# Optimization experiments

Hardware: AMD Instinct MI355X
Metric: run time of the kernel (lower is better)

## Reference

```python
import jax, jax.numpy as jnp
from jax import lax
import numpy as np

VTH = 0.2
DECAY = 0.25            # LIF membrane decay used by pcdmd slayers.LIFSpike (STBP-style)
DT = 0.001              # norse default integration step
TAU_SYN_INV = 200.0     # norse LSNNParameters defaults
TAU_MEM_INV = 100.0
TAU_ADAPT_INV = 1.0 / 700.0
BETA = 0.0              # module sets beta=0 (no threshold adaptation jumps)
ALPHA = 100.0           # SuperSpike surrogate slope (norse 'super' method)

@jax.custom_vjp
def spike_rect(v):
    # Heaviside forward, rectangular surrogate backward (STBP)
    return (v > 0).astype(v.dtype)

def _sr_fwd(v):
    return spike_rect(v), v

def _sr_bwd(v, g):
    return (g * (jnp.abs(v) < 0.5).astype(g.dtype),)

spike_rect.defvjp(_sr_fwd, _sr_bwd)

@jax.custom_vjp
def spike_super(v):
    # Heaviside forward, SuperSpike surrogate backward (norse 'super')
    return (v > 0).astype(v.dtype)

def _ss_fwd(v):
    return spike_super(v), v

def _ss_bwd(v, g):
    return (g / (ALPHA * jnp.abs(v) + 1.0) ** 2,)

spike_super.defvjp(_ss_fwd, _ss_bwd)

def lif_spike(x):
    # x: [..., T] -> spike train [..., T]
    # u_t = DECAY * u_{t-1} * (1 - o_{t-1}) + x_t ; o_t = H(u_t - VTH)
    xT = jnp.moveaxis(x, -1, 0)  # [T, ...]
    u0 = jnp.zeros(xT.shape[1:], x.dtype)
    def step(carry, xt):
        u, o = carry
        u = DECAY * u * (1.0 - o) + xt
        o = spike_rect(u - VTH)
        return (u, o), o
    _, out = lax.scan(step, (u0, u0), xT)
    return jnp.moveaxis(out, 0, -1)

def lsnn_recurrent(x, w_in, w_rec):
    # x: [T, B, H] input spikes; norse LSNNRecurrent lsnn_step with beta=0, v_th=VTH
    x_in = jnp.einsum('tbh,oh->tbo', x, w_in)  # input current, hoisted out of scan
    B, H = x.shape[1], w_in.shape[0]
    z0 = jnp.zeros((B, H), x.dtype)
    state0 = (z0, z0, z0, jnp.full((B, H), VTH, x.dtype))  # z, v, i, b (b starts at v_th)
    def step(state, xt):
        z, v, i, b = state
        i_jump = i + xt + z @ w_rec.T
        v_dec = v + DT * TAU_MEM_INV * (-v + i_jump)          # v_leak = 0
        i_dec = i_jump - DT * TAU_SYN_INV * i_jump
        b_dec = b + DT * TAU_ADAPT_INV * (VTH - b)
        z_new = spike_super(v_dec - b_dec)
        v_new = (1.0 - z_new) * v_dec                          # v_reset = 0
        b_new = b_dec + z_new * TAU_ADAPT_INV * BETA
        return (z_new, v_new, i_dec, b_new), z_new
    _, out = lax.scan(step, state0, x_in)
    return out  # [T, B, H]

def setup_inputs() -> dict:
    key = jax.random.key(0)
    ks = jax.random.split(key, 7)
    B, T = 64, 8192
    EEG_C, AUD_C, H, OUT = 64, 1, 10, 2
    x = jax.random.normal(ks[0], (B, 1, EEG_C + 2 * AUD_C, T), jnp.float32)
    s_in = 1.0 / float(np.sqrt(EEG_C))
    s_h = 1.0 / float(np.sqrt(H))
    return {
        'x': x,
        'w_front': jax.random.uniform(ks[1], (H, EEG_C), jnp.float32, -s_in, s_in),
        'b_front': jax.random.uniform(ks[2], (H,), jnp.float32, -s_in, s_in),
        'w_in': jax.random.uniform(ks[3], (H, H), jnp.float32, -s_h, s_h),
        'w_rec': jax.random.uniform(ks[4], (H, H), jnp.float32, -s_h, s_h),
        'w_cls': jax.random.uniform(ks[5], (OUT, H), jnp.float32, -s_h, s_h),
        'b_cls': jax.random.uniform(ks[6], (OUT,), jnp.float32, -s_h, s_h),
    }

def reference(x, w_front, b_front, w_in, w_rec, w_cls, b_cls):
    AUD_C = 1
    window_length = x.shape[-1]
    eeg = x[:, 0, AUD_C:-AUD_C, :]                              # [B, 64, T]
    eeg = jnp.einsum('bct,hc->bht', eeg, w_front) + b_front[None, :, None]
    eeg = lif_spike(eeg)                                        # spike_tanh in snn mode
    eeg = jnp.transpose(eeg, (2, 0, 1))                         # [T, B, H]
    z = lsnn_recurrent(eeg, w_in, w_rec)                        # [T, B, H]
    out = jnp.transpose(z, (1, 2, 0))                           # [B, H, T]
    out = jnp.einsum('bht,oh->bot', out, w_cls) + b_cls[None, :, None]
    out = lif_spike(out)                                        # spike_sigmoid in snn mode
    return jnp.sum(out, axis=2) / window_length                 # [B, 2]
```

## Files before the change

kernel.cpp:

```cpp
#include <hip/hip_runtime.h>
#include <cstdint>
#include <cstddef>

#define T_LEN 8192
#define BATCH 64
#define HID   10
#define CH    66
#define EEG   64
#define SM_STRIDE 8384

__global__ void k_front(const float* __restrict__ x, const float* __restrict__ wf_g,
                        const float* __restrict__ bf_g, float* __restrict__ y) {
    __shared__ float wf[EEG][HID];
    __shared__ float bf[HID];
    int tid = threadIdx.x;
    for (int i = tid; i < EEG * HID; i += 256) {
        int h = i / EEG, c = i % EEG;
        wf[c][h] = wf_g[i];
    }
    if (tid < HID) bf[tid] = bf_g[tid];
    __syncthreads();

    int b = blockIdx.y;
    int t4 = (blockIdx.x * 256 + tid) * 4;
    const float* xb = x + ((size_t)b * CH + 1) * T_LEN + t4;
    float acc[4][HID];
#pragma unroll
    for (int j = 0; j < 4; ++j)
#pragma unroll
        for (int h = 0; h < HID; ++h) acc[j][h] = bf[h];
#pragma unroll 4
    for (int c = 0; c < EEG; ++c) {
        float4 xv = *(const float4*)(xb + (size_t)c * T_LEN);
#pragma unroll
        for (int h = 0; h < HID; ++h) {
            float w = wf[c][h];
            acc[0][h] = fmaf(xv.x, w, acc[0][h]);
            acc[1][h] = fmaf(xv.y, w, acc[1][h]);
            acc[2][h] = fmaf(xv.z, w, acc[2][h]);
            acc[3][h] = fmaf(xv.w, w, acc[3][h]);
        }
    }
    float* yo = y + (size_t)b * HID * T_LEN + t4;
#pragma unroll
    for (int h = 0; h < HID; ++h)
        *(float4*)(yo + (size_t)h * T_LEN) =
            make_float4(acc[0][h], acc[1][h], acc[2][h], acc[3][h]);
}

__global__ __launch_bounds__(64) void k_flif(const float* __restrict__ y,
                                             unsigned short* __restrict__ smask) {
    int id = blockIdx.x;
    int c  = (id & 7) * 16 + ((id >> 3) & 15);
    int bq = id >> 7;
    int lane = threadIdx.x;
    int g = lane >> 4, h = lane & 15;
    int b = bq * 4 + g;
    int hh = h < HID ? h : HID - 1;

    if (c == 0) {
        for (int i = lane; i < 4 * 96; i += 64) {
            int j = i / 96, w = i % 96;
            ((unsigned*)(smask + (size_t)(bq * 4 + j) * SM_STRIDE))[w] = 0u;
        }
    }

    int t0 = c * 64;
    int ts = t0 - 32; if (ts < 0) ts = 0;
    int nf = (t0 + 64 - ts) >> 2;
    const float4* yb = (const float4*)(y + ((size_t)b * HID + hh) * T_LEN + ts);

    float4 A = yb[0], B = yb[1], C = yb[2];
    float u = 0.f, o = 0.f;
    unsigned short* smb = smask + (size_t)b * SM_STRIDE + 192;
    for (int f = 0; f < nf; ++f) {
        int nx = f + 3; if (nx > nf - 1) nx = nf - 1;
        float4 D = yb[nx];
        float vv[4] = {A.x, A.y, A.z, A.w};
        int tb = ts + f * 4;
#pragma unroll
        for (int k = 0; k < 4; ++k) {
            u = (o > 0.5f) ? vv[k] : fmaf(0.25f, u, vv[k]);
            bool sp = (u > 0.2f);
            o = sp ? 1.0f : 0.0f;
            unsigned long long bal = __ballot(sp);
            int t = tb + k;
            if (t >= t0 && h == 0)
                smb[t] = (unsigned short)((bal >> (g * 16)) & 0x3FFull);
        }
        A = B; B = C; C = D;
    }
}

__global__ __launch_bounds__(512) void k_lsnn(
    const unsigned short* __restrict__ smask,
    const float* __restrict__ w_in, const float* __restrict__ w_rec,
    const float* __restrict__ w_cls, const float* __restrict__ b_cls,
    float* __restrict__ out) {
    extern __shared__ float LDSBUF[];
    float* T = LDSBUF;
    float* D = LDSBUF + 1536;
    int tid = threadIdx.x;
    for (int i = tid; i < 1536; i += 512) {
        int hi = i / 768;
        int rem = i - hi * 768;
        int m = rem / 24, role = rem - m * 24;
        float s = 0.f;
        if (role < 22) {
            const float* wrow = (role < 10) ? (w_in + role * HID)
                              : (role < 12) ? (w_cls + (role - 10) * HID)
                                            : (w_rec + (role - 12) * HID);
#pragma unroll
            for (int j = 0; j < 5; ++j)
                if (m & (1u << j)) s += wrow[hi * 5 + j];
        }
        T[i] = s;
    }
    __syncthreads();
    for (int i = tid; i < 1024 * 22; i += 512) {
        int z = i / 22, role = i - z * 22;
        D[i] = T[(z & 31) * 24 + role] + T[768 + (z >> 5) * 24 + role];
    }
    __syncthreads();

    int lane = tid & 63;
    int q = lane >> 4;
    int r = lane & 15;
    int rr = r < 12 ? r : 11;
    int rrec = 12 + (r < HID ? r : 9);
    int shq = q * 16;
    int id = blockIdx.x * 32 + (tid >> 4);
    int b = id >> 7, chunk = id & 127;

    float bcl = (r == 10 || r == 11) ? b_cls[r - HID] : 0.f;

    const unsigned short* sm = smask + (size_t)b * SM_STRIDE + (size_t)chunk * 64;

    auto xlook = [&](const uint4& mv, float* X) {
        unsigned hw[8] = { mv.x & 0x3FFu, (mv.x >> 16) & 0x3FFu,
                           mv.y & 0x3FFu, (mv.y >> 16) & 0x3FFu,
                           mv.z & 0x3FFu, (mv.z >> 16) & 0x3FFu,
                           mv.w & 0x3FFu, (mv.w >> 16) & 0x3FFu };
#pragma unroll
        for (int u = 0; u < 8; ++u)
            X[u] = D[hw[u] * 22 + rr];
    };

    uint4 mB = *(const uint4*)(sm + 8);
    uint4 mC = *(const uint4*)(sm + 16);
    uint4 mD = *(const uint4*)(sm + 24);
    float Xc[8], Xn[8], Pc[8], Pn[8];
    { uint4 m0 = *(const uint4*)(sm); xlook(m0, Xc); }
#pragma unroll
    for (int u = 0; u < 8; ++u) { Pc[u] = 0.f; Pn[u] = 0.f; }

    float v = 0.f, cur = 0.f;
    unsigned zmask = 0;
    float uc = 0.f, oc = 0.f, accs = 0.f;

    for (int gr = 0; gr < 32; ++gr) {
        int nb = gr + 4; if (nb > 31) nb = 31;
        uint4 mE = *(const uint4*)(sm + (size_t)nb * 8);
        xlook(mB, Xn);
        unsigned zs[8];
#pragma unroll
        for (int u = 0; u < 8; ++u) {
            float rec = D[zmask * 22 + rrec];
            float ij = (cur + Xc[u]) + rec;
            float vd = v + 0.1f * (ij - v);
            cur = ij - 0.2f * ij;
            bool zb = vd > 0.2f;
            unsigned long long bal = __ballot(zb);
            v = zb ? 0.f : vd;
            zmask = (unsigned)(bal >> shq) & 0x3FFu;
            zs[u] = zmask;
        }
        if (gr >= 21) {
#pragma unroll
            for (int u = 0; u < 8; ++u)
                Pn[u] = D[zs[u] * 22 + rr];
        }
        if (gr >= 22) {
            bool in = (gr >= 25);
#pragma unroll
            for (int u = 0; u < 8; ++u) {
                float ci = Pc[u] + bcl;
                uc = (oc > 0.5f) ? ci : fmaf(0.25f, uc, ci);
                oc = (uc > 0.2f) ? 1.f : 0.f;
                if (in) accs += oc;
            }
        }
#pragma unroll
        for (int u = 0; u < 8; ++u) { Xc[u] = Xn[u]; Pc[u] = Pn[u]; }
        mB = mC; mC = mD; mD = mE;
    }
#pragma unroll
    for (int u = 0; u < 8; ++u) {
        float ci = Pc[u] + bcl;
        uc = (oc > 0.5f) ? ci : fmaf(0.25f, uc, ci);
        oc = (uc > 0.2f) ? 1.f : 0.f;
        accs += oc;
    }
    if (r == 10 || r == 11)
        atomicAdd(&out[b * 2 + (r - 10)], accs * (1.0f / 8192.0f));
}

extern "C" void kernel_launch(void* const* d_in, const int* in_sizes, int n_in,
                              void* d_out, int out_size, void* d_ws, size_t ws_size,
                              hipStream_t stream) {
    const float* x       = (const float*)d_in[0];
    const float* w_front = (const float*)d_in[1];
    const float* b_front = (const float*)d_in[2];
    const float* w_in    = (const float*)d_in[3];
    const float* w_rec   = (const float*)d_in[4];
    const float* w_cls   = (const float*)d_in[5];
    const float* b_cls   = (const float*)d_in[6];
    float* out = (float*)d_out;

    float* y = (float*)d_ws;
    unsigned short* smask =
        (unsigned short*)((char*)d_ws + (size_t)BATCH * HID * T_LEN * sizeof(float));

    hipMemsetAsync(out, 0, (size_t)out_size * sizeof(float), stream);
    k_front<<<dim3(T_LEN / 1024, BATCH), 256, 0, stream>>>(x, w_front, b_front, y);
    k_flif<<<dim3(2048), 64, 0, stream>>>(y, smask);
    k_lsnn<<<dim3(256), 512, (1536 + 1024 * 22) * sizeof(float), stream>>>(
        smask, w_in, w_rec, w_cls, b_cls, out);
}
```

Before: 279.5 us.

## Fuse front projection and LIF spiking into one kernel via LDS tile

Merges the front-end channel projection and the first LIF spike kernel into a single kernel. Each block computes a 1024-step time tile, plus a 32-step warm-up halo, of projected currents into shared memory. Four wavefronts then each run the LIF recurrence over 256-step segments and write the spike masks. This removes the global round trip of the intermediate current tensor, the separate memset, and one launch. The costs are a longer serial LIF chain per wave, a second load-imbalanced projection pass for the halo, and higher LDS use per block.

```diff
diff --git a/kernel.cpp b/kernel.cpp
--- a/kernel.cpp
+++ b/kernel.cpp
@@ -8,87 +8,94 @@
 #define CH    66
 #define EEG   64
 #define SM_STRIDE 8384
-
-__global__ void k_front(const float* __restrict__ x, const float* __restrict__ wf_g,
-                        const float* __restrict__ bf_g, float* __restrict__ y) {
+#define TS    1060
+
+__global__ __launch_bounds__(256) void k_front_lif(
+    const float* __restrict__ x, const float* __restrict__ wf_g,
+    const float* __restrict__ bf_g, unsigned short* __restrict__ smask,
+    float* __restrict__ out) {
     __shared__ float wf[EEG][HID];
     __shared__ float bf[HID];
+    __shared__ float yt[HID][TS];
     int tid = threadIdx.x;
     for (int i = tid; i < EEG * HID; i += 256) {
         int h = i / EEG, c = i % EEG;
         wf[c][h] = wf_g[i];
     }
     if (tid < HID) bf[tid] = bf_g[tid];
-    __syncthreads();
-
-    int b = blockIdx.y;
-    int t4 = (blockIdx.x * 256 + tid) * 4;
-    const float* xb = x + ((size_t)b * CH + 1) * T_LEN + t4;
-    float acc[4][HID];
-#pragma unroll
-    for (int j = 0; j < 4; ++j)
-#pragma unroll
-        for (int h = 0; h < HID; ++h) acc[j][h] = bf[h];
+
+    int chunk = blockIdx.x;
+    int b     = blockIdx.y;
+    if (chunk == 0) {
+        for (int i = tid; i < 96; i += 256)
+            ((unsigned*)(smask + (size_t)b * SM_STRIDE))[i] = 0u;
+        if (b == 0)
+            for (int i = tid; i < BATCH * 2; i += 256) out[i] = 0.f;
+    }
+    __syncthreads();
+
+    int t0 = chunk * 1024;
+    const float* xb = x + ((size_t)b * CH + 1) * T_LEN;
+    for (int g = tid; g < 264; g += 256) {
+        int t = t0 - 32 + 4 * g;
+        if (t < 0) continue;
+        float acc[4][HID];
+#pragma unroll
+        for (int j = 0; j < 4; ++j)
+#pragma unroll
+            for (int h = 0; h < HID; ++h) acc[j][h] = bf[h];
+        const float* xp = xb + t;
 #pragma unroll 4
-    for (int c = 0; c < EEG; ++c) {
-        float4 xv = *(const float4*)(xb + (size_t)c * T_LEN);
-#pragma unroll
-        for (int h = 0; h < HID; ++h) {
-            float w = wf[c][h];
-            acc[0][h] = fmaf(xv.x, w, acc[0][h]);
-            acc[1][h] = fmaf(xv.y, w, acc[1][h]);
-            acc[2][h] = fmaf(xv.z, w, acc[2][h]);
-            acc[3][h] = fmaf(xv.w, w, acc[3][h]);
-        }
-    }
-    float* yo = y + (size_t)b * HID * T_LEN + t4;
-#pragma unroll
-    for (int h = 0; h < HID; ++h)
-        *(float4*)(yo + (size_t)h * T_LEN) =
-            make_float4(acc[0][h], acc[1][h], acc[2][h], acc[3][h]);
-}
-
-__global__ __launch_bounds__(64) void k_flif(const float* __restrict__ y,
-                                             unsigned short* __restrict__ smask) {
-    int id = blockIdx.x;
-    int c  = (id & 7) * 16 + ((id >> 3) & 15);
-    int bq = id >> 7;
-    int lane = threadIdx.x;
-    int g = lane >> 4, h = lane & 15;
-    int b = bq * 4 + g;
-    int hh = h < HID ? h : HID - 1;
-
-    if (c == 0) {
-        for (int i = lane; i < 4 * 96; i += 64) {
-            int j = i / 96, w = i % 96;
-            ((unsigned*)(smask + (size_t)(bq * 4 + j) * SM_STRIDE))[w] = 0u;
-        }
-    }
-
-    int t0 = c * 64;
-    int ts = t0 - 32; if (ts < 0) ts = 0;
-    int nf = (t0 + 64 - ts) >> 2;
-    const float4* yb = (const float4*)(y + ((size_t)b * HID + hh) * T_LEN + ts);
-
-    float4 A = yb[0], B = yb[1], C = yb[2];
+        for (int c = 0; c < EEG; ++c) {
+            float4 xv = *(const float4*)(xp + (size_t)c * T_LEN);
+#pragma unroll
+            for (int h = 0; h < HID; ++h) {
+                float w = wf[c][h];
+                acc[0][h] = fmaf(xv.x, w, acc[0][h]);
+                acc[1][h] = fmaf(xv.y, w, acc[1][h]);
+                acc[2][h] = fmaf(xv.z, w, acc[2][h]);
+                acc[3][h] = fmaf(xv.w, w, acc[3][h]);
+            }
+        }
+        int k = 4 * g;
+#pragma unroll
+        for (int h = 0; h < HID; ++h)
+            *(float4*)&yt[h][k] =
+                make_float4(acc[0][h], acc[1][h], acc[2][h], acc[3][h]);
+    }
+    __syncthreads();
+
+    int w    = tid >> 6;
+    int lane = tid & 63;
+    int h    = lane & 15;
+    int hh   = h < HID ? h : HID - 1;
+
+    int kliv = 32 + 256 * w;
+    int wl   = (chunk == 0 && w == 0) ? 0 : 32;
+    int ks   = kliv - wl;
+    int nf   = (256 + wl) >> 2;
+    const float4* yrow = (const float4*)&yt[hh][0];
+    int base = ks >> 2;
+
+    unsigned short* smb = smask + (size_t)b * SM_STRIDE + 192 + t0 + 256 * w;
     float u = 0.f, o = 0.f;
-    unsigned short* smb = smask + (size_t)b * SM_STRIDE + 192;
+    float4 A = yrow[base], B = yrow[base + 1];
     for (int f = 0; f < nf; ++f) {
-        int nx = f + 3; if (nx > nf - 1) nx = nf - 1;
-        float4 D = yb[nx];
+        int nx = f + 2; if (nx > nf - 1) nx = nf - 1;
+        float4 C = yrow[base + nx];
         float vv[4] = {A.x, A.y, A.z, A.w};
-        int tb = ts + f * 4;
-#pragma unroll
-        for (int k = 0; k < 4; ++k) {
-            u = (o > 0.5f) ? vv[k] : fmaf(0.25f, u, vv[k]);
+        int kb = ks + 4 * f;
+#pragma unroll
+        for (int k2 = 0; k2 < 4; ++k2) {
+            u = (o > 0.5f) ? vv[k2] : fmaf(0.25f, u, vv[k2]);
             bool sp = (u > 0.2f);
             o = sp ? 1.0f : 0.0f;
             unsigned long long bal = __ballot(sp);
-            int t = tb + k;
-            if (t >= t0 && h == 0)
-                smb[t] = (unsigned short)((bal >> (g * 16)) & 0x3FFull);
-        }
-        A = B; B = C; C = D;
+            int k = kb + k2;
+            if (k >= kliv && h == 0)
+                smb[k - kliv] = (unsigned short)(bal & 0x3FFull);
+        }
+        A = B; B = C;
     }
 }
 
@@ -217,13 +224,9 @@
     const float* b_cls   = (const float*)d_in[6];
     float* out = (float*)d_out;
 
-    float* y = (float*)d_ws;
-    unsigned short* smask =
-        (unsigned short*)((char*)d_ws + (size_t)BATCH * HID * T_LEN * sizeof(float));
-
-    hipMemsetAsync(out, 0, (size_t)out_size * sizeof(float), stream);
-    k_front<<<dim3(T_LEN / 1024, BATCH), 256, 0, stream>>>(x, w_front, b_front, y);
-    k_flif<<<dim3(2048), 64, 0, stream>>>(y, smask);
+    unsigned short* smask = (unsigned short*)d_ws;
+
+    k_front_lif<<<dim3(8, BATCH), 256, 0, stream>>>(x, w_front, b_front, smask, out);
     k_lsnn<<<dim3(256), 512, (1536 + 1024 * 22) * sizeof(float), stream>>>(
         smask, w_in, w_rec, w_cls, b_cls, out);
 }
```

Result: no change. 277.6 us (-0.7%).
